# Optimization experiments

Measured on AMD Instinct MI355X. Metric: run time of the kernel, lower is better.

Reference implementation:

```python
import jax, jax.numpy as jnp
import numpy as np

B, C, E = 4, 2048, 1024
H, D = 16, 64


def setup_inputs() -> dict:
    key = jax.random.key(0)
    kx, kq, kk, kv, ko = jax.random.split(key, 5)
    s = 0.02
    return {
        "x": jax.random.normal(kx, (B, C, E), dtype=jnp.float32),
        "W_q": jax.random.normal(kq, (E, H * D), dtype=jnp.float32) * s,
        "W_k": jax.random.normal(kk, (E, H * D), dtype=jnp.float32) * s,
        "W_v": jax.random.normal(kv, (E, H * D), dtype=jnp.float32) * s,
        "W_o": jax.random.normal(ko, (H * D, E), dtype=jnp.float32) * s,
    }


def reference(x, W_q, W_k, W_v, W_o):
    b, c, e = x.shape
    # projections -> [B, H, C, D]
    def split_heads(t):
        return t.reshape(b, c, H, D).transpose(0, 2, 1, 3)
    Q = split_heads(x @ W_q)
    K = split_heads(x @ W_k)
    V = split_heads(x @ W_v)
    scale = 1.0 / jnp.sqrt(jnp.asarray(D, dtype=x.dtype))
    scores = jnp.einsum("bhqd,bhkd->bhqk", Q, K) * scale  # [B,H,C,C]
    causal = jnp.tril(jnp.ones((c, c), dtype=bool))
    scores = jnp.where(causal, scores, jnp.asarray(-jnp.inf, dtype=scores.dtype))
    weights = jax.nn.softmax(scores, axis=-1)
    hidden = jnp.einsum("bhqk,bhkd->bhqd", weights, V)  # [B,H,C,D]
    hidden = hidden.transpose(0, 2, 1, 3).reshape(b, c, H * D)
    return hidden @ W_o
```

## Files before the change

### kernel.cpp

```cpp
#include <hip/hip_runtime.h>

typedef __bf16 bf16;
typedef __attribute__((ext_vector_type(8))) __bf16 bf16x8;
typedef __attribute__((ext_vector_type(4))) __bf16 bf16x4;
typedef __attribute__((ext_vector_type(4))) float f32x4;
typedef __attribute__((ext_vector_type(16))) float f32x16;

#define B_ 4
#define C_ 2048
#define E_ 1024
#define H_ 16
#define D_ 64

__device__ __forceinline__ void gload16(const void* g, void* l) {
  __builtin_amdgcn_global_load_lds(
      (const __attribute__((address_space(1))) void*)g,
      (__attribute__((address_space(3))) void*)l, 16, 0, 0);
}

__device__ __forceinline__ unsigned cvtpk(float lo, float hi) {
  unsigned r;
  asm("v_cvt_pk_bf16_f32 %0, %1, %2" : "=v"(r) : "v"(lo), "v"(hi));
  return r;
}
__device__ __forceinline__ void pswap(unsigned& a, unsigned& b) {
  asm volatile("v_permlane32_swap_b32 %0, %1" : "+v"(a), "+v"(b));
}
__device__ __forceinline__ bf16x8 mkfrag(unsigned d0, unsigned d1, unsigned d2,
                                         unsigned d3) {
  union {
    unsigned u[4];
    bf16x8 v;
  } x;
  x.u[0] = d0;
  x.u[1] = d1;
  x.u[2] = d2;
  x.u[3] = d3;
  return x.v;
}

__global__ __launch_bounds__(256) void xconv(const float* __restrict__ x,
                                             bf16* __restrict__ xb) {
  const size_t i = (size_t)blockIdx.x * 256 + threadIdx.x;
  const float4* p = (const float4*)(x + i * 8);
  float4 a = p[0], b = p[1];
  bf16x8 v = {(__bf16)a.x, (__bf16)a.y, (__bf16)a.z, (__bf16)a.w,
              (__bf16)b.x, (__bf16)b.y, (__bf16)b.z, (__bf16)b.w};
  *(bf16x8*)(xb + i * 8) = v;
}

__global__ __launch_bounds__(256) void wtrans(const float* __restrict__ Wq,
                                              const float* __restrict__ Wk,
                                              const float* __restrict__ Wv,
                                              const float* __restrict__ Wo,
                                              bf16* __restrict__ WT) {
  const float* W = blockIdx.z == 0 ? Wq : blockIdx.z == 1 ? Wk
                 : blockIdx.z == 2 ? Wv : Wo;
  bf16* dst = WT + (size_t)blockIdx.z * 1024 * 1024;
  __shared__ bf16 t[64][65];
  const int tx = threadIdx.x & 63, ty = threadIdx.x >> 6;
  const int r0 = blockIdx.y * 64, c0 = blockIdx.x * 64;
#pragma unroll
  for (int r = ty; r < 64; r += 4)
    t[tx][r] = (__bf16)W[(size_t)(r0 + r) * 1024 + c0 + tx];
  __syncthreads();
#pragma unroll
  for (int r = ty; r < 64; r += 4)
    dst[(size_t)(c0 + r) * 1024 + r0 + tx] = t[r][tx];
}

template <int MODE>
__global__ __launch_bounds__(256, 2) void gemm_bt(const bf16* __restrict__ A,
                                                  const bf16* __restrict__ WTall,
                                                  bf16* __restrict__ Qo,
                                                  bf16* __restrict__ Ko,
                                                  bf16* __restrict__ Vto,
                                                  float* __restrict__ Fo) {
  constexpr int BK = 64;
  constexpr int NT = 1024 / BK;
  const int tid = threadIdx.x;
  const int wave = tid >> 6, lane = tid & 63;
  const int cl = lane & 15, g = lane >> 4;
  const int wr = wave >> 1, wc = wave & 1;
  const int brow = blockIdx.x * 128;
  const int bcol = blockIdx.y * 128;
  const bf16* Bt =
      (MODE == 0) ? (WTall + (size_t)blockIdx.z * 1024 * 1024) : WTall;

  __shared__ __align__(16) bf16 ldsA[2][128 * BK];
  __shared__ __align__(16) bf16 ldsB[2][128 * BK];

  f32x4 acc[4][4] = {};

  auto STAGE = [&](int kt, int buf) {
#pragma unroll
    for (int it = 0; it < 4; ++it) {
      const int chunk = it * 256 + tid;
      const int row = chunk >> 3, slot = chunk & 7;
      const int se = (slot ^ (row & 7)) * 8;
      const int ldsoff = (it * 256 + wave * 64) * 16;
      gload16(A + (size_t)(brow + row) * 1024 + kt + se,
              (char*)&ldsA[buf][0] + ldsoff);
      gload16(Bt + (size_t)(bcol + row) * 1024 + kt + se,
              (char*)&ldsB[buf][0] + ldsoff);
    }
  };

  STAGE(0, 0);
  STAGE(BK, 1);
  asm volatile("s_waitcnt vmcnt(8)" ::: "memory");
  __builtin_amdgcn_s_barrier();

  for (int t = 0; t < NT; ++t) {
    const int buf = t & 1;
    bf16x8 af[2][4], bfr[2][4];
#pragma unroll
    for (int kkid = 0; kkid < 2; ++kkid) {
#pragma unroll
      for (int i = 0; i < 4; ++i) {
        const int sl = ((4 * kkid + g) ^ (cl & 7)) * 8;
        af[kkid][i] = *(const bf16x8*)&ldsA[buf][(wr * 64 + i * 16 + cl) * BK + sl];
        bfr[kkid][i] = *(const bf16x8*)&ldsB[buf][(wc * 64 + i * 16 + cl) * BK + sl];
      }
    }
    asm volatile("s_waitcnt lgkmcnt(0)" ::: "memory");
    __builtin_amdgcn_sched_barrier(0);
    __builtin_amdgcn_s_barrier();

    if (t + 2 < NT) STAGE((t + 2) * BK, buf);

#pragma unroll
    for (int kkid = 0; kkid < 2; ++kkid)
#pragma unroll
      for (int i = 0; i < 4; ++i)
#pragma unroll
        for (int j = 0; j < 4; ++j)
          acc[i][j] = __builtin_amdgcn_mfma_f32_16x16x32_bf16(
              af[kkid][i], bfr[kkid][j], acc[i][j], 0, 0, 0);

    if (t + 2 < NT)
      asm volatile("s_waitcnt vmcnt(8)" ::: "memory");
    else
      asm volatile("s_waitcnt vmcnt(0)" ::: "memory");
    __builtin_amdgcn_s_barrier();
  }

  bf16* dst = nullptr;
  if constexpr (MODE == 0)
    dst = blockIdx.z == 0 ? Qo : blockIdx.z == 1 ? Ko : Vto;
  const float presc =
      (MODE == 0 && blockIdx.z == 0) ? 0.18033688011112042f : 1.0f;
#pragma unroll
  for (int i = 0; i < 4; ++i) {
#pragma unroll
    for (int j = 0; j < 4; ++j) {
#pragma unroll
      for (int r = 0; r < 4; ++r) {
        const int gr = brow + wr * 64 + i * 16 + g * 4 + r;
        const int gc = bcol + wc * 64 + j * 16 + cl;
        const float v = acc[i][j][r] * presc;
        if constexpr (MODE == 0) {
          const int b = gr >> 11, c = gr & 2047;
          const int h = gc >> 6, d = gc & 63;
          if (blockIdx.z == 2)
            dst[(((size_t)b * H_ + h) * D_ + d) * C_ + c] = (__bf16)v;
          else
            dst[(((size_t)b * H_ + h) * C_ + c) * D_ + d] = (__bf16)v;
        } else {
          Fo[(size_t)gr * 1024 + gc] = v;
        }
      }
    }
  }
}

__device__ __forceinline__ void sm_fixed(f32x16& s0, f32x16& s1, f32x4& l4,
                                         int th0, bool domask, int hi,
                                         bf16x8& pf0, bf16x8& pf1,
                                         bf16x8& pf2, bf16x8& pf3) {
  if (domask) {
#pragma unroll
    for (int r = 0; r < 16; ++r) {
      const int crow = (r & 3) + 8 * (r >> 2) + 4 * hi;
      if (crow > th0) s0[r] = -1e30f;
      if (crow + 32 > th0) s1[r] = -1e30f;
    }
  }
#pragma unroll
  for (int r = 0; r < 16; ++r) {
    s0[r] = __builtin_amdgcn_exp2f(s0[r]);
    s1[r] = __builtin_amdgcn_exp2f(s1[r]);
  }
#pragma unroll
  for (int r = 0; r < 16; ++r) l4[r & 3] += s0[r] + s1[r];
  unsigned a0 = cvtpk(s0[0], s0[1]), a1 = cvtpk(s0[2], s0[3]);
  unsigned b0 = cvtpk(s0[4], s0[5]), b1 = cvtpk(s0[6], s0[7]);
  unsigned c0 = cvtpk(s0[8], s0[9]), c1 = cvtpk(s0[10], s0[11]);
  unsigned d0 = cvtpk(s0[12], s0[13]), d1 = cvtpk(s0[14], s0[15]);
  unsigned e0 = cvtpk(s1[0], s1[1]), e1 = cvtpk(s1[2], s1[3]);
  unsigned f0 = cvtpk(s1[4], s1[5]), f1 = cvtpk(s1[6], s1[7]);
  unsigned g0 = cvtpk(s1[8], s1[9]), g1 = cvtpk(s1[10], s1[11]);
  unsigned h0 = cvtpk(s1[12], s1[13]), h1 = cvtpk(s1[14], s1[15]);
  pswap(a0, b0);
  pswap(a1, b1);
  pswap(c0, d0);
  pswap(c1, d1);
  pswap(e0, f0);
  pswap(e1, f1);
  pswap(g0, h0);
  pswap(g1, h1);
  pf0 = mkfrag(a0, a1, b0, b1);
  pf1 = mkfrag(c0, c1, d0, d1);
  pf2 = mkfrag(e0, e1, f0, f1);
  pf3 = mkfrag(g0, g1, h0, h1);
}

__global__ __launch_bounds__(256, 2) void attn(const bf16* __restrict__ Qg,
                                               const bf16* __restrict__ Kg,
                                               const bf16* __restrict__ Vt,
                                               bf16* __restrict__ Hid) {
  const int tid = threadIdx.x, wave = tid >> 6, lane = tid & 63;
  const int l31 = lane & 31, hi = lane >> 5, l7 = lane & 7;
  const int qa = blockIdx.x, qb = 15 - (int)blockIdx.x;
  const int h = blockIdx.y, b = blockIdx.z;
  const size_t bh = (size_t)b * H_ + h;

  __shared__ __align__(16) bf16 ldsK[2 * 64 * 64];
  __shared__ __align__(16) bf16 ldsV[2 * 64 * 64];

  const bf16* Kb = Kg + bh * C_ * D_;
  const bf16* Vb = Vt + bh * (size_t)D_ * C_;

  const int qrowA = qa * 128 + wave * 32;
  const int qrowB = qb * 128 + wave * 32;

  bf16x8 qfA[4], qfB[4];
  {
    const bf16* qra = Qg + (bh * C_ + qrowA + l31) * D_;
    const bf16* qrb = Qg + (bh * C_ + qrowB + l31) * D_;
#pragma unroll
    for (int ds = 0; ds < 4; ++ds) {
      qfA[ds] = *(const bf16x8*)(qra + ds * 16 + 8 * hi);
      qfB[ds] = *(const bf16x8*)(qrb + ds * 16 + 8 * hi);
    }
  }

  f32x4 l4A = {}, l4B = {};
  f32x16 oA0 = {}, oA1 = {}, oB0 = {}, oB1 = {};

  auto STAGE = [&](int kt, int buf) {
#pragma unroll
    for (int it = 0; it < 2; ++it) {
      const int chunk = it * 256 + tid;
      const int row = chunk >> 3, slot = chunk & 7;
      const int se = (slot ^ (row & 7)) * 8;
      const int ldsoff = buf * 8192 + (it * 256 + wave * 64) * 16;
      gload16(Kb + (size_t)kt * 64 * D_ + row * 64 + se, (char*)ldsK + ldsoff);
      gload16(Vb + (size_t)row * C_ + kt * 64 + se, (char*)ldsV + ldsoff);
    }
  };

  const int last = 2 * qb + 1;
  STAGE(0, 0);

  for (int kt = 0; kt <= last; ++kt) {
    const int cur = kt & 1;
    const bf16* kb = ldsK + cur * 4096;
    const bf16* vb = ldsV + cur * 4096;
    if (kt < last) {
      STAGE(kt + 1, cur ^ 1);
      asm volatile("s_waitcnt vmcnt(4)" ::: "memory");
    } else {
      asm volatile("s_waitcnt vmcnt(0)" ::: "memory");
    }
    __builtin_amdgcn_s_barrier();
    __builtin_amdgcn_sched_barrier(0);

    const bool actA = (kt * 64 <= qrowA + 31);
    const bool actB = (kt * 64 <= qrowB + 31);

    f32x16 sA0 = {}, sA1 = {}, sB0 = {}, sB1 = {};
    __builtin_amdgcn_s_setprio(1);
#pragma unroll
    for (int ds = 0; ds < 4; ++ds) {
      const int sl = ((2 * ds + hi) ^ l7) * 8;
      bf16x8 kf0 = *(const bf16x8*)&kb[l31 * 64 + sl];
      bf16x8 kf1 = *(const bf16x8*)&kb[(32 + l31) * 64 + sl];
      if (actA) {
        sA0 = __builtin_amdgcn_mfma_f32_32x32x16_bf16(kf0, qfA[ds], sA0, 0, 0, 0);
        sA1 = __builtin_amdgcn_mfma_f32_32x32x16_bf16(kf1, qfA[ds], sA1, 0, 0, 0);
      }
      if (actB) {
        sB0 = __builtin_amdgcn_mfma_f32_32x32x16_bf16(kf0, qfB[ds], sB0, 0, 0, 0);
        sB1 = __builtin_amdgcn_mfma_f32_32x32x16_bf16(kf1, qfB[ds], sB1, 0, 0, 0);
      }
    }
    __builtin_amdgcn_s_setprio(0);

    bf16x8 vf0[4], vf1[4];
#pragma unroll
    for (int ks = 0; ks < 4; ++ks) {
      const int sl = ((2 * ks + hi) ^ l7) * 8;
      vf0[ks] = *(const bf16x8*)&vb[l31 * 64 + sl];
      vf1[ks] = *(const bf16x8*)&vb[(32 + l31) * 64 + sl];
    }

    if (actA) {
      bf16x8 p0, p1, p2, p3;
      sm_fixed(sA0, sA1, l4A, qrowA + l31 - kt * 64, kt * 64 + 63 > qrowA, hi,
               p0, p1, p2, p3);
      __builtin_amdgcn_s_setprio(1);
      oA0 = __builtin_amdgcn_mfma_f32_32x32x16_bf16(vf0[0], p0, oA0, 0, 0, 0);
      oA1 = __builtin_amdgcn_mfma_f32_32x32x16_bf16(vf1[0], p0, oA1, 0, 0, 0);
      oA0 = __builtin_amdgcn_mfma_f32_32x32x16_bf16(vf0[1], p1, oA0, 0, 0, 0);
      oA1 = __builtin_amdgcn_mfma_f32_32x32x16_bf16(vf1[1], p1, oA1, 0, 0, 0);
      oA0 = __builtin_amdgcn_mfma_f32_32x32x16_bf16(vf0[2], p2, oA0, 0, 0, 0);
      oA1 = __builtin_amdgcn_mfma_f32_32x32x16_bf16(vf1[2], p2, oA1, 0, 0, 0);
      oA0 = __builtin_amdgcn_mfma_f32_32x32x16_bf16(vf0[3], p3, oA0, 0, 0, 0);
      oA1 = __builtin_amdgcn_mfma_f32_32x32x16_bf16(vf1[3], p3, oA1, 0, 0, 0);
      __builtin_amdgcn_s_setprio(0);
    }
    if (actB) {
      bf16x8 p0, p1, p2, p3;
      sm_fixed(sB0, sB1, l4B, qrowB + l31 - kt * 64, kt * 64 + 63 > qrowB, hi,
               p0, p1, p2, p3);
      __builtin_amdgcn_s_setprio(1);
      oB0 = __builtin_amdgcn_mfma_f32_32x32x16_bf16(vf0[0], p0, oB0, 0, 0, 0);
      oB1 = __builtin_amdgcn_mfma_f32_32x32x16_bf16(vf1[0], p0, oB1, 0, 0, 0);
      oB0 = __builtin_amdgcn_mfma_f32_32x32x16_bf16(vf0[1], p1, oB0, 0, 0, 0);
      oB1 = __builtin_amdgcn_mfma_f32_32x32x16_bf16(vf1[1], p1, oB1, 0, 0, 0);
      oB0 = __builtin_amdgcn_mfma_f32_32x32x16_bf16(vf0[2], p2, oB0, 0, 0, 0);
      oB1 = __builtin_amdgcn_mfma_f32_32x32x16_bf16(vf1[2], p2, oB1, 0, 0, 0);
      oB0 = __builtin_amdgcn_mfma_f32_32x32x16_bf16(vf0[3], p3, oB0, 0, 0, 0);
      oB1 = __builtin_amdgcn_mfma_f32_32x32x16_bf16(vf1[3], p3, oB1, 0, 0, 0);
      __builtin_amdgcn_s_setprio(0);
    }
    __builtin_amdgcn_s_barrier();
  }

#pragma unroll
  for (int st = 0; st < 2; ++st) {
    const f32x4 l4 = st ? l4B : l4A;
    float l = (l4[0] + l4[1]) + (l4[2] + l4[3]);
    l += __shfl_xor(l, 32, 64);
    const float inv = 1.0f / l;
    const int qrow = st ? qrowB : qrowA;
    const size_t row = (size_t)b * C_ + qrow + l31;
#pragma unroll
    for (int dt = 0; dt < 2; ++dt) {
      const f32x16& oo = st ? (dt ? oB1 : oB0) : (dt ? oA1 : oA0);
#pragma unroll
      for (int q4 = 0; q4 < 4; ++q4) {
        bf16x4 pk = {(__bf16)(oo[4 * q4 + 0] * inv),
                     (__bf16)(oo[4 * q4 + 1] * inv),
                     (__bf16)(oo[4 * q4 + 2] * inv),
                     (__bf16)(oo[4 * q4 + 3] * inv)};
        const int d = dt * 32 + 8 * q4 + 4 * hi;
        *(bf16x4*)&Hid[row * (H_ * D_) + h * 64 + d] = pk;
      }
    }
  }
}

extern "C" void kernel_launch(void* const* d_in, const int* in_sizes, int n_in,
                              void* d_out, int out_size, void* d_ws,
                              size_t ws_size, hipStream_t stream) {
  const float* x = (const float*)d_in[0];
  const float* Wq = (const float*)d_in[1];
  const float* Wk = (const float*)d_in[2];
  const float* Wv = (const float*)d_in[3];
  const float* Wo = (const float*)d_in[4];

  char* ws = (char*)d_ws;
  bf16* xb = (bf16*)ws;
  bf16* WT = (bf16*)(ws + (16ull << 20));
  bf16* Qb = (bf16*)(ws + (24ull << 20));
  bf16* Kb = (bf16*)(ws + (40ull << 20));
  bf16* Vtb = (bf16*)(ws + (56ull << 20));
  bf16* Hid = (bf16*)(ws + (72ull << 20));

  xconv<<<dim3(4096), 256, 0, stream>>>(x, xb);
  wtrans<<<dim3(16, 16, 4), 256, 0, stream>>>(Wq, Wk, Wv, Wo, WT);
  gemm_bt<0><<<dim3(64, 8, 3), 256, 0, stream>>>(xb, WT, Qb, Kb, Vtb, nullptr);
  attn<<<dim3(8, H_, B_), 256, 0, stream>>>(Qb, Kb, Vtb, Hid);
  gemm_bt<1><<<dim3(64, 8, 1), 256, 0, stream>>>(
      Hid, WT + 3ull * 1024 * 1024, nullptr, nullptr, nullptr, (float*)d_out);
}
```

Baseline: 160.4 us.

## Merge prep kernels and stage 128-key KV tiles in attention

The x conversion and weight transpose kernels are merged into one launch, with blocks split by blockIdx.z, to save one kernel launch. In attention, each pipeline stage now loads 128 keys of K and V instead of 64, and processes them as two 64-key halves. This halves the number of barriers and wait points per key-value sweep. In exchange, LDS use doubles to 64KB per block, which may limit occupancy, and there is some extra index arithmetic for the swizzled addressing.

```diff
diff --git a/kernel.cpp b/kernel.cpp
--- a/kernel.cpp
+++ b/kernel.cpp
@@ -39,34 +39,37 @@
   return x.v;
 }
 
-__global__ __launch_bounds__(256) void xconv(const float* __restrict__ x,
-                                             bf16* __restrict__ xb) {
-  const size_t i = (size_t)blockIdx.x * 256 + threadIdx.x;
-  const float4* p = (const float4*)(x + i * 8);
-  float4 a = p[0], b = p[1];
-  bf16x8 v = {(__bf16)a.x, (__bf16)a.y, (__bf16)a.z, (__bf16)a.w,
-              (__bf16)b.x, (__bf16)b.y, (__bf16)b.z, (__bf16)b.w};
-  *(bf16x8*)(xb + i * 8) = v;
-}
-
-__global__ __launch_bounds__(256) void wtrans(const float* __restrict__ Wq,
-                                              const float* __restrict__ Wk,
-                                              const float* __restrict__ Wv,
-                                              const float* __restrict__ Wo,
-                                              bf16* __restrict__ WT) {
-  const float* W = blockIdx.z == 0 ? Wq : blockIdx.z == 1 ? Wk
-                 : blockIdx.z == 2 ? Wv : Wo;
-  bf16* dst = WT + (size_t)blockIdx.z * 1024 * 1024;
-  __shared__ bf16 t[64][65];
-  const int tx = threadIdx.x & 63, ty = threadIdx.x >> 6;
-  const int r0 = blockIdx.y * 64, c0 = blockIdx.x * 64;
-#pragma unroll
-  for (int r = ty; r < 64; r += 4)
-    t[tx][r] = (__bf16)W[(size_t)(r0 + r) * 1024 + c0 + tx];
-  __syncthreads();
-#pragma unroll
-  for (int r = ty; r < 64; r += 4)
-    dst[(size_t)(c0 + r) * 1024 + r0 + tx] = t[r][tx];
+__global__ __launch_bounds__(256) void prep(const float* __restrict__ x,
+                                            const float* __restrict__ Wq,
+                                            const float* __restrict__ Wk,
+                                            const float* __restrict__ Wv,
+                                            const float* __restrict__ Wo,
+                                            bf16* __restrict__ xb,
+                                            bf16* __restrict__ WT) {
+  if (blockIdx.z < 4) {
+    const float* W = blockIdx.z == 0 ? Wq : blockIdx.z == 1 ? Wk
+                   : blockIdx.z == 2 ? Wv : Wo;
+    bf16* dst = WT + (size_t)blockIdx.z * 1024 * 1024;
+    __shared__ bf16 t[64][65];
+    const int tx = threadIdx.x & 63, ty = threadIdx.x >> 6;
+    const int r0 = blockIdx.y * 64, c0 = blockIdx.x * 64;
+#pragma unroll
+    for (int r = ty; r < 64; r += 4)
+      t[tx][r] = (__bf16)W[(size_t)(r0 + r) * 1024 + c0 + tx];
+    __syncthreads();
+#pragma unroll
+    for (int r = ty; r < 64; r += 4)
+      dst[(size_t)(c0 + r) * 1024 + r0 + tx] = t[r][tx];
+  } else {
+    const size_t chunk =
+        ((size_t)(blockIdx.z - 4) * 256 + blockIdx.y * 16 + blockIdx.x);
+    const size_t i = chunk * 256 + threadIdx.x;
+    const float4* p = (const float4*)(x + i * 8);
+    float4 a = p[0], b = p[1];
+    bf16x8 v = {(__bf16)a.x, (__bf16)a.y, (__bf16)a.z, (__bf16)a.w,
+                (__bf16)b.x, (__bf16)b.y, (__bf16)b.z, (__bf16)b.w};
+    *(bf16x8*)(xb + i * 8) = v;
+  }
 }
 
 template <int MODE>
@@ -225,8 +228,8 @@
   const int h = blockIdx.y, b = blockIdx.z;
   const size_t bh = (size_t)b * H_ + h;
 
-  __shared__ __align__(16) bf16 ldsK[2 * 64 * 64];
-  __shared__ __align__(16) bf16 ldsV[2 * 64 * 64];
+  __shared__ __align__(16) bf16 ldsK[2 * 128 * 64];
+  __shared__ __align__(16) bf16 ldsV[2 * 64 * 128];
 
   const bf16* Kb = Kg + bh * C_ * D_;
   const bf16* Vb = Vt + bh * (size_t)D_ * C_;
@@ -250,90 +253,102 @@
 
   auto STAGE = [&](int kt, int buf) {
 #pragma unroll
-    for (int it = 0; it < 2; ++it) {
-      const int chunk = it * 256 + tid;
-      const int row = chunk >> 3, slot = chunk & 7;
-      const int se = (slot ^ (row & 7)) * 8;
-      const int ldsoff = buf * 8192 + (it * 256 + wave * 64) * 16;
-      gload16(Kb + (size_t)kt * 64 * D_ + row * 64 + se, (char*)ldsK + ldsoff);
-      gload16(Vb + (size_t)row * C_ + kt * 64 + se, (char*)ldsV + ldsoff);
+    for (int w = 0; w < 4; ++w) {
+      const int chunk = w * 256 + tid;
+      {
+        const int row = chunk >> 3, slot = chunk & 7;
+        const int se = (slot ^ (row & 7)) * 8;
+        gload16(Kb + ((size_t)kt * 128 + row) * D_ + se,
+                (char*)ldsK + buf * 16384 + (w * 256 + wave * 64) * 16);
+      }
+      {
+        const int row = chunk >> 4, slot = chunk & 15;
+        const int se = (slot ^ (row & 7)) * 8;
+        gload16(Vb + (size_t)row * C_ + kt * 128 + se,
+                (char*)ldsV + buf * 16384 + (w * 256 + wave * 64) * 16);
+      }
     }
   };
 
-  const int last = 2 * qb + 1;
+  const int nkv = qb + 1;
   STAGE(0, 0);
 
-  for (int kt = 0; kt <= last; ++kt) {
+  for (int kt = 0; kt < nkv; ++kt) {
     const int cur = kt & 1;
-    const bf16* kb = ldsK + cur * 4096;
-    const bf16* vb = ldsV + cur * 4096;
-    if (kt < last) {
+    const bf16* kb = ldsK + cur * 8192;
+    const bf16* vb = ldsV + cur * 8192;
+    if (kt + 1 < nkv) {
       STAGE(kt + 1, cur ^ 1);
-      asm volatile("s_waitcnt vmcnt(4)" ::: "memory");
+      asm volatile("s_waitcnt vmcnt(8)" ::: "memory");
     } else {
       asm volatile("s_waitcnt vmcnt(0)" ::: "memory");
     }
     __builtin_amdgcn_s_barrier();
     __builtin_amdgcn_sched_barrier(0);
 
-    const bool actA = (kt * 64 <= qrowA + 31);
-    const bool actB = (kt * 64 <= qrowB + 31);
-
-    f32x16 sA0 = {}, sA1 = {}, sB0 = {}, sB1 = {};
-    __builtin_amdgcn_s_setprio(1);
-#pragma unroll
-    for (int ds = 0; ds < 4; ++ds) {
-      const int sl = ((2 * ds + hi) ^ l7) * 8;
-      bf16x8 kf0 = *(const bf16x8*)&kb[l31 * 64 + sl];
-      bf16x8 kf1 = *(const bf16x8*)&kb[(32 + l31) * 64 + sl];
+#pragma unroll
+    for (int hh = 0; hh < 2; ++hh) {
+      const int key0 = kt * 128 + hh * 64;
+      const bool actA = (key0 <= qrowA + 31);
+      const bool actB = (key0 <= qrowB + 31);
+      if (!actA && !actB) continue;
+
+      f32x16 sA0 = {}, sA1 = {}, sB0 = {}, sB1 = {};
+      __builtin_amdgcn_s_setprio(1);
+#pragma unroll
+      for (int ds = 0; ds < 4; ++ds) {
+        const int r0 = hh * 64 + l31, r1 = hh * 64 + 32 + l31;
+        bf16x8 kf0 = *(const bf16x8*)&kb[r0 * 64 + (((2 * ds + hi) ^ (r0 & 7)) * 8)];
+        bf16x8 kf1 = *(const bf16x8*)&kb[r1 * 64 + (((2 * ds + hi) ^ (r1 & 7)) * 8)];
+        if (actA) {
+          sA0 = __builtin_amdgcn_mfma_f32_32x32x16_bf16(kf0, qfA[ds], sA0, 0, 0, 0);
+          sA1 = __builtin_amdgcn_mfma_f32_32x32x16_bf16(kf1, qfA[ds], sA1, 0, 0, 0);
+        }
+        if (actB) {
+          sB0 = __builtin_amdgcn_mfma_f32_32x32x16_bf16(kf0, qfB[ds], sB0, 0, 0, 0);
+          sB1 = __builtin_amdgcn_mfma_f32_32x32x16_bf16(kf1, qfB[ds], sB1, 0, 0, 0);
+        }
+      }
+      __builtin_amdgcn_s_setprio(0);
+
+      bf16x8 vf0[4], vf1[4];
+#pragma unroll
+      for (int ks = 0; ks < 4; ++ks) {
+        const int gs = hh * 8 + 2 * ks + hi;
+        vf0[ks] = *(const bf16x8*)&vb[l31 * 128 + ((gs ^ (l31 & 7)) * 8)];
+        vf1[ks] = *(const bf16x8*)&vb[(32 + l31) * 128 + ((gs ^ ((32 + l31) & 7)) * 8)];
+      }
+
       if (actA) {
-        sA0 = __builtin_amdgcn_mfma_f32_32x32x16_bf16(kf0, qfA[ds], sA0, 0, 0, 0);
-        sA1 = __builtin_amdgcn_mfma_f32_32x32x16_bf16(kf1, qfA[ds], sA1, 0, 0, 0);
+        bf16x8 p0, p1, p2, p3;
+        sm_fixed(sA0, sA1, l4A, qrowA + l31 - key0, key0 + 63 > qrowA, hi,
+                 p0, p1, p2, p3);
+        __builtin_amdgcn_s_setprio(1);
+        oA0 = __builtin_amdgcn_mfma_f32_32x32x16_bf16(vf0[0], p0, oA0, 0, 0, 0);
+        oA1 = __builtin_amdgcn_mfma_f32_32x32x16_bf16(vf1[0], p0, oA1, 0, 0, 0);
+        oA0 = __builtin_amdgcn_mfma_f32_32x32x16_bf16(vf0[1], p1, oA0, 0, 0, 0);
+        oA1 = __builtin_amdgcn_mfma_f32_32x32x16_bf16(vf1[1], p1, oA1, 0, 0, 0);
+        oA0 = __builtin_amdgcn_mfma_f32_32x32x16_bf16(vf0[2], p2, oA0, 0, 0, 0);
+        oA1 = __builtin_amdgcn_mfma_f32_32x32x16_bf16(vf1[2], p2, oA1, 0, 0, 0);
+        oA0 = __builtin_amdgcn_mfma_f32_32x32x16_bf16(vf0[3], p3, oA0, 0, 0, 0);
+        oA1 = __builtin_amdgcn_mfma_f32_32x32x16_bf16(vf1[3], p3, oA1, 0, 0, 0);
+        __builtin_amdgcn_s_setprio(0);
       }
       if (actB) {
-        sB0 = __builtin_amdgcn_mfma_f32_32x32x16_bf16(kf0, qfB[ds], sB0, 0, 0, 0);
-        sB1 = __builtin_amdgcn_mfma_f32_32x32x16_bf16(kf1, qfB[ds], sB1, 0, 0, 0);
-      }
-    }
-    __builtin_amdgcn_s_setprio(0);
-
-    bf16x8 vf0[4], vf1[4];
-#pragma unroll
-    for (int ks = 0; ks < 4; ++ks) {
-      const int sl = ((2 * ks + hi) ^ l7) * 8;
-      vf0[ks] = *(const bf16x8*)&vb[l31 * 64 + sl];
-      vf1[ks] = *(const bf16x8*)&vb[(32 + l31) * 64 + sl];
-    }
-
-    if (actA) {
-      bf16x8 p0, p1, p2, p3;
-      sm_fixed(sA0, sA1, l4A, qrowA + l31 - kt * 64, kt * 64 + 63 > qrowA, hi,
-               p0, p1, p2, p3);
-      __builtin_amdgcn_s_setprio(1);
-      oA0 = __builtin_amdgcn_mfma_f32_32x32x16_bf16(vf0[0], p0, oA0, 0, 0, 0);
-      oA1 = __builtin_amdgcn_mfma_f32_32x32x16_bf16(vf1[0], p0, oA1, 0, 0, 0);
-      oA0 = __builtin_amdgcn_mfma_f32_32x32x16_bf16(vf0[1], p1, oA0, 0, 0, 0);
-      oA1 = __builtin_amdgcn_mfma_f32_32x32x16_bf16(vf1[1], p1, oA1, 0, 0, 0);
-      oA0 = __builtin_amdgcn_mfma_f32_32x32x16_bf16(vf0[2], p2, oA0, 0, 0, 0);
-      oA1 = __builtin_amdgcn_mfma_f32_32x32x16_bf16(vf1[2], p2, oA1, 0, 0, 0);
-      oA0 = __builtin_amdgcn_mfma_f32_32x32x16_bf16(vf0[3], p3, oA0, 0, 0, 0);
-      oA1 = __builtin_amdgcn_mfma_f32_32x32x16_bf16(vf1[3], p3, oA1, 0, 0, 0);
-      __builtin_amdgcn_s_setprio(0);
-    }
-    if (actB) {
-      bf16x8 p0, p1, p2, p3;
-      sm_fixed(sB0, sB1, l4B, qrowB + l31 - kt * 64, kt * 64 + 63 > qrowB, hi,
-               p0, p1, p2, p3);
-      __builtin_amdgcn_s_setprio(1);
-      oB0 = __builtin_amdgcn_mfma_f32_32x32x16_bf16(vf0[0], p0, oB0, 0, 0, 0);
-      oB1 = __builtin_amdgcn_mfma_f32_32x32x16_bf16(vf1[0], p0, oB1, 0, 0, 0);
-      oB0 = __builtin_amdgcn_mfma_f32_32x32x16_bf16(vf0[1], p1, oB0, 0, 0, 0);
-      oB1 = __builtin_amdgcn_mfma_f32_32x32x16_bf16(vf1[1], p1, oB1, 0, 0, 0);
-      oB0 = __builtin_amdgcn_mfma_f32_32x32x16_bf16(vf0[2], p2, oB0, 0, 0, 0);
-      oB1 = __builtin_amdgcn_mfma_f32_32x32x16_bf16(vf1[2], p2, oB1, 0, 0, 0);
-      oB0 = __builtin_amdgcn_mfma_f32_32x32x16_bf16(vf0[3], p3, oB0, 0, 0, 0);
-      oB1 = __builtin_amdgcn_mfma_f32_32x32x16_bf16(vf1[3], p3, oB1, 0, 0, 0);
-      __builtin_amdgcn_s_setprio(0);
+        bf16x8 p0, p1, p2, p3;
+        sm_fixed(sB0, sB1, l4B, qrowB + l31 - key0, key0 + 63 > qrowB, hi,
+                 p0, p1, p2, p3);
+        __builtin_amdgcn_s_setprio(1);
+        oB0 = __builtin_amdgcn_mfma_f32_32x32x16_bf16(vf0[0], p0, oB0, 0, 0, 0);
+        oB1 = __builtin_amdgcn_mfma_f32_32x32x16_bf16(vf1[0], p0, oB1, 0, 0, 0);
+        oB0 = __builtin_amdgcn_mfma_f32_32x32x16_bf16(vf0[1], p1, oB0, 0, 0, 0);
+        oB1 = __builtin_amdgcn_mfma_f32_32x32x16_bf16(vf1[1], p1, oB1, 0, 0, 0);
+        oB0 = __builtin_amdgcn_mfma_f32_32x32x16_bf16(vf0[2], p2, oB0, 0, 0, 0);
+        oB1 = __builtin_amdgcn_mfma_f32_32x32x16_bf16(vf1[2], p2, oB1, 0, 0, 0);
+        oB0 = __builtin_amdgcn_mfma_f32_32x32x16_bf16(vf0[3], p3, oB0, 0, 0, 0);
+        oB1 = __builtin_amdgcn_mfma_f32_32x32x16_bf16(vf1[3], p3, oB1, 0, 0, 0);
+        __builtin_amdgcn_s_setprio(0);
+      }
     }
     __builtin_amdgcn_s_barrier();
   }
@@ -379,8 +394,7 @@
   bf16* Vtb = (bf16*)(ws + (56ull << 20));
   bf16* Hid = (bf16*)(ws + (72ull << 20));
 
-  xconv<<<dim3(4096), 256, 0, stream>>>(x, xb);
-  wtrans<<<dim3(16, 16, 4), 256, 0, stream>>>(Wq, Wk, Wv, Wo, WT);
+  prep<<<dim3(16, 16, 20), 256, 0, stream>>>(x, Wq, Wk, Wv, Wo, xb, WT);
   gemm_bt<0><<<dim3(64, 8, 3), 256, 0, stream>>>(xb, WT, Qb, Kb, Vtb, nullptr);
   attn<<<dim3(8, H_, B_), 256, 0, stream>>>(Qb, Kb, Vtb, Hid);
   gemm_bt<1><<<dim3(64, 8, 1), 256, 0, stream>>>(
```

After: 157.5 us. About the same (-1.8%).
